# Optimization experiments

Measured on AMD Instinct MI355X. Metric: run time of the kernel, lower is better.

Reference implementation:

```python
import jax, jax.numpy as jnp
import numpy as np

EMBED_DIM = 512
NUM_HEADS = 8
HEAD_DIM = EMBED_DIM // NUM_HEADS


def setup_inputs() -> dict:
    key = jax.random.key(0)
    kx, kq, kk, kv, ko = jax.random.split(key, 5)
    B, T, C = 2, 4096, EMBED_DIM
    s = 1.0 / np.sqrt(C)  # torch Linear default init scale (uniform); use scaled normal
    return {
        "x": jax.random.normal(kx, (B, T, C), dtype=jnp.float32),
        "Wq": jax.random.normal(kq, (C, C), dtype=jnp.float32) * s,
        "Wk": jax.random.normal(kk, (C, C), dtype=jnp.float32) * s,
        "Wv": jax.random.normal(kv, (C, C), dtype=jnp.float32) * s,
        "Wo": jax.random.normal(ko, (C, C), dtype=jnp.float32) * s,
    }


def reference(x, Wq, Wk, Wv, Wo):
    B, T, C = x.shape
    H, D = NUM_HEADS, HEAD_DIM

    def split_heads(t):
        return t.reshape(B, T, H, D).transpose(0, 2, 1, 3)  # [B,H,T,D]

    # nn.Linear: y = x @ W^T
    Q = split_heads(x @ Wq.T)
    K = split_heads(x @ Wk.T)
    V = split_heads(x @ Wv.T)

    scale = jnp.sqrt(jnp.asarray(D, dtype=x.dtype))
    scores = jnp.einsum("bhqd,bhkd->bhqk", Q, K) / scale  # [B,H,T,T]
    causal = jnp.tril(jnp.ones((T, T), dtype=bool))
    scores = jnp.where(causal, scores, -jnp.inf)
    weights = jax.nn.softmax(scores, axis=-1)
    out = jnp.einsum("bhqk,bhkd->bhqd", weights, V)  # [B,H,T,D]
    out = out.transpose(0, 2, 1, 3).reshape(B, T, C)
    return out @ Wo.T
```

## Files before the change

### kernel.cpp

```cpp
#include <hip/hip_runtime.h>
#include <stdint.h>

#define B_DIM 2
#define T_DIM 4096
#define C_DIM 512
#define H_DIM 8
#define D_DIM 64
#define M_DIM (B_DIM * T_DIM)

typedef __attribute__((ext_vector_type(8))) short bf16x8;
typedef __attribute__((ext_vector_type(4))) float f32x4;
typedef __attribute__((ext_vector_type(4))) short short4v;

__device__ inline unsigned short f2bf(float f) {
    union { float f; uint32_t u; } v; v.f = f;
    uint32_t r = v.u + 0x7fffu + ((v.u >> 16) & 1u);
    return (unsigned short)(r >> 16);
}

__device__ inline uint32_t cvtpk(float a, float b) {
    uint32_t r;
    asm("v_cvt_pk_bf16_f32 %0, %1, %2" : "=v"(r) : "v"(a), "v"(b));
    return r;
}

__device__ inline float fexp2(float x) {
    float r;
    asm("v_exp_f32 %0, %1" : "=v"(r) : "v"(x));
    return r;
}

__device__ inline float bf2f(unsigned short u) {
    union { uint32_t u; float f; } v; v.u = (uint32_t)u << 16; return v.f;
}

__global__ __launch_bounds__(256) void cvt_kernel(const float* __restrict__ in,
                                                  unsigned short* __restrict__ out, int n) {
    int i = (blockIdx.x * 256 + threadIdx.x) * 4;
    if (i >= n) return;
    float4 v = *(const float4*)(in + i);
    uint2 o;
    o.x = cvtpk(v.x, v.y);
    o.y = cvtpk(v.z, v.w);
    *(uint2*)(out + i) = o;
}

__global__ __launch_bounds__(256) void cvt_w_kernel(const float* __restrict__ Wq,
                                                    const float* __restrict__ Wk,
                                                    const float* __restrict__ Wv,
                                                    const float* __restrict__ Wo,
                                                    unsigned short* __restrict__ out) {
    const int widx = blockIdx.x >> 8;
    const float* src = (widx == 0) ? Wq : (widx == 1) ? Wk : (widx == 2) ? Wv : Wo;
    const int i = ((blockIdx.x & 255) * 256 + threadIdx.x) * 4;
    float4 v = *(const float4*)(src + i);
    uint2 o;
    o.x = cvtpk(v.x, v.y);
    o.y = cvtpk(v.z, v.w);
    *(uint2*)(out + (size_t)widx * C_DIM * C_DIM + i) = o;
}

__global__ __launch_bounds__(256, 2) void gemm_qkv(const unsigned short* __restrict__ A,
                                                   const unsigned short* __restrict__ Wb,
                                                   unsigned short* __restrict__ Qh,
                                                   unsigned short* __restrict__ Kh,
                                                   unsigned short* __restrict__ Vt) {
    const int tid  = threadIdx.x;
    const int wave = tid >> 6;
    const int lane = tid & 63;
    const int g    = lane >> 4;
    const int lr   = lane & 15;
    const int rowB = blockIdx.x * 128;
    const int col0 = blockIdx.y * 128;
    const int z    = blockIdx.z;
    const unsigned short* W = Wb + (size_t)z * C_DIM * C_DIM;

    __shared__ unsigned short As[2][128][40];
    __shared__ unsigned short Bs[2][128][40];

    const int sr = tid >> 1;
    const int sc = (tid & 1) * 16;

    f32x4 acc[2][8];
#pragma unroll
    for (int r = 0; r < 2; ++r)
#pragma unroll
        for (int i = 0; i < 8; ++i) acc[r][i] = (f32x4){0.f, 0.f, 0.f, 0.f};

    const unsigned short* Ag = A + (size_t)(rowB + sr) * C_DIM + sc;
    const unsigned short* Bg = W + (size_t)(col0 + sr) * C_DIM + sc;

    *(bf16x8*)&As[0][sr][sc]     = *(const bf16x8*)(Ag);
    *(bf16x8*)&As[0][sr][sc + 8] = *(const bf16x8*)(Ag + 8);
    *(bf16x8*)&Bs[0][sr][sc]     = *(const bf16x8*)(Bg);
    *(bf16x8*)&Bs[0][sr][sc + 8] = *(const bf16x8*)(Bg + 8);
    __syncthreads();

    int cur = 0;
#pragma unroll 1
    for (int kk = 0; kk < C_DIM; kk += 32) {
        const bool hn = (kk + 32 < C_DIM);
        bf16x8 na0, na1, nb0, nb1;
        if (hn) {
            na0 = *(const bf16x8*)(Ag + kk + 32);
            na1 = *(const bf16x8*)(Ag + kk + 40);
            nb0 = *(const bf16x8*)(Bg + kk + 32);
            nb1 = *(const bf16x8*)(Bg + kk + 40);
        }

        bf16x8 a0 = *(const bf16x8*)&As[cur][wave * 32 + lr][g * 8];
        bf16x8 a1 = *(const bf16x8*)&As[cur][wave * 32 + 16 + lr][g * 8];
#pragma unroll
        for (int nt = 0; nt < 8; ++nt) {
            bf16x8 b = *(const bf16x8*)&Bs[cur][nt * 16 + lr][g * 8];
            acc[0][nt] = __builtin_amdgcn_mfma_f32_16x16x32_bf16(a0, b, acc[0][nt], 0, 0, 0);
            acc[1][nt] = __builtin_amdgcn_mfma_f32_16x16x32_bf16(a1, b, acc[1][nt], 0, 0, 0);
        }

        if (hn) {
            *(bf16x8*)&As[cur ^ 1][sr][sc]     = na0;
            *(bf16x8*)&As[cur ^ 1][sr][sc + 8] = na1;
            *(bf16x8*)&Bs[cur ^ 1][sr][sc]     = nb0;
            *(bf16x8*)&Bs[cur ^ 1][sr][sc + 8] = nb1;
        }
        __syncthreads();
        cur ^= 1;
    }

    const int row0 = rowB + wave * 32;
    unsigned short* Oqk = (z == 0) ? Qh : Kh;
#pragma unroll
    for (int ar = 0; ar < 2; ++ar) {
        const int rowb = row0 + ar * 16;
#pragma unroll
        for (int nt = 0; nt < 8; ++nt) {
            const int n = col0 + nt * 16 + lr;
            const int h = n >> 6, d = n & 63;
            if (z < 2) {
#pragma unroll
                for (int j = 0; j < 4; ++j) {
                    int m = rowb + g * 4 + j;
                    int b = m >> 12, t = m & (T_DIM - 1);
                    Oqk[((size_t)(b * H_DIM + h) * T_DIM + t) * D_DIM + d] = f2bf(acc[ar][nt][j]);
                }
            } else {
                int m = rowb + g * 4;
                int b = m >> 12, t = m & (T_DIM - 1);
                int tp = (t & ~31) | (((t >> 2) & 3) << 3) | (((t >> 4) & 1) << 2);
                short4v pack;
#pragma unroll
                for (int j = 0; j < 4; ++j) pack[j] = (short)f2bf(acc[ar][nt][j]);
                *(short4v*)(Vt + ((size_t)(b * H_DIM + h) * D_DIM + d) * T_DIM + tp) = pack;
            }
        }
    }
}

__global__ __launch_bounds__(256, 2) void gemm_out(const unsigned short* __restrict__ A,
                                                   const unsigned short* __restrict__ W,
                                                   float* __restrict__ O) {
    const int tid  = threadIdx.x;
    const int wave = tid >> 6;
    const int lane = tid & 63;
    const int g    = lane >> 4;
    const int lr   = lane & 15;
    const int rowB = blockIdx.x * 128;
    const int col0 = blockIdx.y * 128;

    __shared__ unsigned short As[2][128][40];
    __shared__ unsigned short Bs[2][128][40];

    const int sr = tid >> 1;
    const int sc = (tid & 1) * 16;

    f32x4 acc[2][8];
#pragma unroll
    for (int r = 0; r < 2; ++r)
#pragma unroll
        for (int i = 0; i < 8; ++i) acc[r][i] = (f32x4){0.f, 0.f, 0.f, 0.f};

    const unsigned short* Ag = A + (size_t)(rowB + sr) * C_DIM + sc;
    const unsigned short* Bg = W + (size_t)(col0 + sr) * C_DIM + sc;

    *(bf16x8*)&As[0][sr][sc]     = *(const bf16x8*)(Ag);
    *(bf16x8*)&As[0][sr][sc + 8] = *(const bf16x8*)(Ag + 8);
    *(bf16x8*)&Bs[0][sr][sc]     = *(const bf16x8*)(Bg);
    *(bf16x8*)&Bs[0][sr][sc + 8] = *(const bf16x8*)(Bg + 8);
    __syncthreads();

    int cur = 0;
#pragma unroll 1
    for (int kk = 0; kk < C_DIM; kk += 32) {
        const bool hn = (kk + 32 < C_DIM);
        bf16x8 na0, na1, nb0, nb1;
        if (hn) {
            na0 = *(const bf16x8*)(Ag + kk + 32);
            na1 = *(const bf16x8*)(Ag + kk + 40);
            nb0 = *(const bf16x8*)(Bg + kk + 32);
            nb1 = *(const bf16x8*)(Bg + kk + 40);
        }

        bf16x8 a0 = *(const bf16x8*)&As[cur][wave * 32 + lr][g * 8];
        bf16x8 a1 = *(const bf16x8*)&As[cur][wave * 32 + 16 + lr][g * 8];
#pragma unroll
        for (int nt = 0; nt < 8; ++nt) {
            bf16x8 b = *(const bf16x8*)&Bs[cur][nt * 16 + lr][g * 8];
            acc[0][nt] = __builtin_amdgcn_mfma_f32_16x16x32_bf16(a0, b, acc[0][nt], 0, 0, 0);
            acc[1][nt] = __builtin_amdgcn_mfma_f32_16x16x32_bf16(a1, b, acc[1][nt], 0, 0, 0);
        }

        if (hn) {
            *(bf16x8*)&As[cur ^ 1][sr][sc]     = na0;
            *(bf16x8*)&As[cur ^ 1][sr][sc + 8] = na1;
            *(bf16x8*)&Bs[cur ^ 1][sr][sc]     = nb0;
            *(bf16x8*)&Bs[cur ^ 1][sr][sc + 8] = nb1;
        }
        __syncthreads();
        cur ^= 1;
    }

    const int row0 = rowB + wave * 32;
#pragma unroll
    for (int ar = 0; ar < 2; ++ar) {
        const int rowb = row0 + ar * 16;
#pragma unroll
        for (int nt = 0; nt < 8; ++nt) {
            const int n = col0 + nt * 16 + lr;
#pragma unroll
            for (int j = 0; j < 4; ++j) {
                int m = rowb + g * 4 + j;
                O[(size_t)m * C_DIM + n] = acc[ar][nt][j];
            }
        }
    }
}

__global__ __launch_bounds__(256, 2) void attn_lds(const unsigned short* __restrict__ Qh,
                                                   const unsigned short* __restrict__ Kh,
                                                   const unsigned short* __restrict__ Vt,
                                                   unsigned short* __restrict__ pO,
                                                   float* __restrict__ pl) {
    const int tid  = threadIdx.x;
    const int wave = tid >> 6;
    const int lane = tid & 63;
    const int g    = lane >> 4;
    const int lr   = lane & 15;
    const int srow = (tid >> 3) & 31;
    const int scol = (tid & 7) * 8;
    const int bid  = blockIdx.x;
    const int bh   = bid & 15;
    const int half = (bid >> 4) & 1;
    const int pr   = bid >> 5;

    const unsigned short* Qp = Qh + (size_t)bh * T_DIM * D_DIM;
    const unsigned short* Kp = Kh + (size_t)bh * T_DIM * D_DIM;
    const unsigned short* Vp = Vt + (size_t)bh * D_DIM * T_DIM;

    const float KC = 0.125f * 1.44269504f;
    const short oneb = (short)0x3F80;
    const bf16x8 ones = {oneb, oneb, oneb, oneb, oneb, oneb, oneb, oneb};

    __shared__ unsigned short Kb[2][2][64][72];
    __shared__ unsigned short Vb[2][2][64][72];

#pragma unroll 1
    for (int t = 0; t < 2; ++t) {
        const int qt = t ? (31 - pr) : pr;
        const int qw = qt * 128 + wave * 32;
        const int kvend_w = qw + 32;
        const int kvend_b = qt * 128 + 128;
        const int kvstart = half * 128;

        bf16x8 qf[2][2];
#pragma unroll
        for (int h = 0; h < 2; ++h)
#pragma unroll
            for (int dh = 0; dh < 2; ++dh)
                qf[h][dh] = *(const bf16x8*)(Qp + (size_t)(qw + h * 16 + lr) * D_DIM + dh * 32 + g * 8);

        f32x4 oacc[2][4];
        f32x4 o5[2];
#pragma unroll
        for (int h = 0; h < 2; ++h) {
#pragma unroll
            for (int d0 = 0; d0 < 4; ++d0) oacc[h][d0] = (f32x4){0.f, 0.f, 0.f, 0.f};
            o5[h] = (f32x4){0.f, 0.f, 0.f, 0.f};
        }

#pragma unroll
        for (int s = 0; s < 2; ++s) {
            const int kb = kvstart + s * 64;
            const unsigned short* Ks = Kp + (size_t)(kb + srow) * D_DIM + scol;
            bf16x8 k0 = *(const bf16x8*)(Ks);
            bf16x8 k1 = *(const bf16x8*)(Ks + 32 * D_DIM);
            const unsigned short* Vs = Vp + (size_t)srow * T_DIM + kb + scol;
            bf16x8 v0 = *(const bf16x8*)(Vs);
            bf16x8 v1 = *(const bf16x8*)(Vs + 32 * T_DIM);
            *(bf16x8*)&Kb[0][s][srow][scol]      = k0;
            *(bf16x8*)&Kb[0][s][srow + 32][scol] = k1;
            *(bf16x8*)&Vb[0][s][srow][scol]      = v0;
            *(bf16x8*)&Vb[0][s][srow + 32][scol] = v1;
        }
        __syncthreads();

        int cur = 0;
#pragma unroll 1
        for (int kv0 = kvstart; kv0 < kvend_b; kv0 += 256) {
            const int kvn = kv0 + 256;
            const bool hn = kvn < kvend_b;

            bf16x8 gk[2][2], gv[2][2];
            if (hn) {
#pragma unroll
                for (int s = 0; s < 2; ++s) {
                    const int kb = kvn + s * 64;
                    const unsigned short* Ks = Kp + (size_t)(kb + srow) * D_DIM + scol;
                    gk[s][0] = *(const bf16x8*)(Ks);
                    gk[s][1] = *(const bf16x8*)(Ks + 32 * D_DIM);
                    const unsigned short* Vs = Vp + (size_t)srow * T_DIM + kb + scol;
                    gv[s][0] = *(const bf16x8*)(Vs);
                    gv[s][1] = *(const bf16x8*)(Vs + 32 * T_DIM);
                }
            }

#pragma unroll 1
            for (int sub = 0; sub < 2; ++sub) {
                const int kvu = kv0 + sub * 64;
                if (kvu < kvend_w) {
                    bf16x8 kc8[4][2], vf[2][4];
#pragma unroll
                    for (int i = 0; i < 4; ++i)
#pragma unroll
                        for (int dh = 0; dh < 2; ++dh)
                            kc8[i][dh] = *(const bf16x8*)&Kb[cur][sub][i * 16 + lr][dh * 32 + g * 8];
#pragma unroll
                    for (int kh = 0; kh < 2; ++kh)
#pragma unroll
                        for (int d0 = 0; d0 < 4; ++d0)
                            vf[kh][d0] = *(const bf16x8*)&Vb[cur][sub][d0 * 16 + lr][kh * 32 + g * 8];

                    f32x4 s[2][4];
#pragma unroll
                    for (int h = 0; h < 2; ++h)
#pragma unroll
                        for (int i = 0; i < 4; ++i) s[h][i] = (f32x4){0.f, 0.f, 0.f, 0.f};
#pragma unroll
                    for (int i = 0; i < 4; ++i) {
                        s[0][i] = __builtin_amdgcn_mfma_f32_16x16x32_bf16(kc8[i][0], qf[0][0], s[0][i], 0, 0, 0);
                        s[0][i] = __builtin_amdgcn_mfma_f32_16x16x32_bf16(kc8[i][1], qf[0][1], s[0][i], 0, 0, 0);
                        s[1][i] = __builtin_amdgcn_mfma_f32_16x16x32_bf16(kc8[i][0], qf[1][0], s[1][i], 0, 0, 0);
                        s[1][i] = __builtin_amdgcn_mfma_f32_16x16x32_bf16(kc8[i][1], qf[1][1], s[1][i], 0, 0, 0);
                    }

                    const bool maskit = (kvu + 63 > qw);
#pragma unroll
                    for (int h = 0; h < 2; ++h) {
                        const int qh = qw + h * 16 + lr;
                        float p[16];
                        if (maskit) {
#pragma unroll
                            for (int i = 0; i < 4; ++i)
#pragma unroll
                                for (int j = 0; j < 4; ++j) {
                                    int kva = kvu + i * 16 + g * 4 + j;
                                    float zz = (kva > qh) ? -1e30f : s[h][i][j];
                                    p[i * 4 + j] = fexp2(zz * KC);
                                }
                        } else {
#pragma unroll
                            for (int i = 0; i < 4; ++i)
#pragma unroll
                                for (int j = 0; j < 4; ++j)
                                    p[i * 4 + j] = fexp2(s[h][i][j] * KC);
                        }

                        union { bf16x8 v; uint32_t w[4]; } pf0, pf1;
#pragma unroll
                        for (int w = 0; w < 4; ++w) pf0.w[w] = cvtpk(p[2 * w], p[2 * w + 1]);
#pragma unroll
                        for (int w = 0; w < 4; ++w) pf1.w[w] = cvtpk(p[8 + 2 * w], p[9 + 2 * w]);

#pragma unroll
                        for (int d0 = 0; d0 < 4; ++d0)
                            oacc[h][d0] = __builtin_amdgcn_mfma_f32_16x16x32_bf16(vf[0][d0], pf0.v, oacc[h][d0], 0, 0, 0);
                        o5[h] = __builtin_amdgcn_mfma_f32_16x16x32_bf16(ones, pf0.v, o5[h], 0, 0, 0);
#pragma unroll
                        for (int d0 = 0; d0 < 4; ++d0)
                            oacc[h][d0] = __builtin_amdgcn_mfma_f32_16x16x32_bf16(vf[1][d0], pf1.v, oacc[h][d0], 0, 0, 0);
                        o5[h] = __builtin_amdgcn_mfma_f32_16x16x32_bf16(ones, pf1.v, o5[h], 0, 0, 0);
                    }
                }
            }

            if (hn) {
#pragma unroll
                for (int s = 0; s < 2; ++s) {
                    *(bf16x8*)&Kb[cur ^ 1][s][srow][scol]      = gk[s][0];
                    *(bf16x8*)&Kb[cur ^ 1][s][srow + 32][scol] = gk[s][1];
                    *(bf16x8*)&Vb[cur ^ 1][s][srow][scol]      = gv[s][0];
                    *(bf16x8*)&Vb[cur ^ 1][s][srow + 32][scol] = gv[s][1];
                }
            }
            __syncthreads();
            cur ^= 1;
        }

        const size_t hb = ((size_t)(half * 16 + bh)) * T_DIM;
#pragma unroll
        for (int h = 0; h < 2; ++h) {
            const int row = qw + h * 16 + lr;
            unsigned short* orow = pO + (hb + row) * D_DIM;
#pragma unroll
            for (int d0 = 0; d0 < 4; ++d0) {
                uint2 st;
                st.x = cvtpk(oacc[h][d0][0], oacc[h][d0][1]);
                st.y = cvtpk(oacc[h][d0][2], oacc[h][d0][3]);
                *(uint2*)(orow + d0 * 16 + g * 4) = st;
            }
            if (g == 0) pl[hb + row] = o5[h][0];
        }
        __syncthreads();
    }
}

__global__ __launch_bounds__(256) void attn_merge(const unsigned short* __restrict__ pO,
                                                  const float* __restrict__ pl,
                                                  unsigned short* __restrict__ attnb) {
    const int c = blockIdx.x * 256 + threadIdx.x;
    const int row = c >> 3;
    const int d = (c & 7) * 8;
    const int bh = row >> 12, r = row & 4095;
    const size_t HS = (size_t)16 * T_DIM * D_DIM;

    const size_t pbase = (size_t)row * D_DIM + d;
    bf16x8 a = *(const bf16x8*)(pO + pbase);
    bf16x8 b = *(const bf16x8*)(pO + HS + pbase);
    const float inv = 1.0f / (pl[row] + pl[(HS / D_DIM) + row]);

    union { bf16x8 v; uint32_t w[4]; } o;
#pragma unroll
    for (int i = 0; i < 4; ++i) {
        float e0 = (bf2f((unsigned short)a[2 * i])     + bf2f((unsigned short)b[2 * i]))     * inv;
        float e1 = (bf2f((unsigned short)a[2 * i + 1]) + bf2f((unsigned short)b[2 * i + 1])) * inv;
        o.w[i] = cvtpk(e0, e1);
    }
    const int bb = bh >> 3, hh = bh & 7;
    *(bf16x8*)(attnb + ((size_t)(bb * T_DIM + r)) * C_DIM + hh * D_DIM + d) = o.v;
}

extern "C" void kernel_launch(void* const* d_in, const int* in_sizes, int n_in,
                              void* d_out, int out_size, void* d_ws, size_t ws_size,
                              hipStream_t stream) {
    const float* x  = (const float*)d_in[0];
    const float* Wq = (const float*)d_in[1];
    const float* Wk = (const float*)d_in[2];
    const float* Wv = (const float*)d_in[3];
    const float* Wo = (const float*)d_in[4];

    char* ws = (char*)d_ws;
    unsigned short* xb    = (unsigned short*)(ws + 0);
    unsigned short* Wb    = (unsigned short*)(ws + 8388608);
    unsigned short* Qh    = (unsigned short*)(ws + 10485760);
    unsigned short* Kh    = (unsigned short*)(ws + 18874368);
    unsigned short* Vt    = (unsigned short*)(ws + 27262976);
    unsigned short* attnb = (unsigned short*)(ws + 35651584);
    unsigned short* pO    = (unsigned short*)(ws + 44040192);
    float*          pl    = (float*)         (ws + 60817408);

    const int nX = M_DIM * C_DIM;

    cvt_kernel<<<nX / 4 / 256, 256, 0, stream>>>(x, xb, nX);
    cvt_w_kernel<<<1024, 256, 0, stream>>>(Wq, Wk, Wv, Wo, Wb);

    dim3 gq(M_DIM / 128, C_DIM / 128, 3);
    gemm_qkv<<<gq, 256, 0, stream>>>(xb, Wb, Qh, Kh, Vt);

    attn_lds<<<512, 256, 0, stream>>>(Qh, Kh, Vt, pO, pl);
    attn_merge<<<2048, 256, 0, stream>>>(pO, pl, attnb);

    gemm_out<<<dim3(M_DIM / 128, C_DIM / 128), 256, 0, stream>>>(attnb, Wb + 3 * C_DIM * C_DIM, (float*)d_out);
}
```

Baseline: 98.35 us.

## Fuse split-KV merge into output GEMM and prescale Q by softmax constant

Removes the separate attn_merge kernel. gemm_out now reads both partial attention outputs and their row sums, normalises them and converts to bf16 while loading its A tiles, which removes one launch and an intermediate buffer round-trip. The softmax scale times log2(e) is also folded into Q at projection time, saving a multiply per score in the attention loop. In exchange, the merge work is repeated across the four column blocks of gemm_out, adding redundant global reads of pO and pl. Rounding Q after scaling also changes bf16 precision slightly.

```diff
diff --git a/kernel.cpp b/kernel.cpp
--- a/kernel.cpp
+++ b/kernel.cpp
@@ -33,6 +33,8 @@
 __device__ inline float bf2f(unsigned short u) {
     union { uint32_t u; float f; } v; v.u = (uint32_t)u << 16; return v.f;
 }
+
+#define KCONST 0.1803368801111204f
 
 __global__ __launch_bounds__(256) void cvt_kernel(const float* __restrict__ in,
                                                   unsigned short* __restrict__ out, int n) {
@@ -129,6 +131,7 @@
 
     const int row0 = rowB + wave * 32;
     unsigned short* Oqk = (z == 0) ? Qh : Kh;
+    const float qs = (z == 0) ? KCONST : 1.0f;
 #pragma unroll
     for (int ar = 0; ar < 2; ++ar) {
         const int rowb = row0 + ar * 16;
@@ -141,7 +144,7 @@
                 for (int j = 0; j < 4; ++j) {
                     int m = rowb + g * 4 + j;
                     int b = m >> 12, t = m & (T_DIM - 1);
-                    Oqk[((size_t)(b * H_DIM + h) * T_DIM + t) * D_DIM + d] = f2bf(acc[ar][nt][j]);
+                    Oqk[((size_t)(b * H_DIM + h) * T_DIM + t) * D_DIM + d] = f2bf(acc[ar][nt][j] * qs);
                 }
             } else {
                 int m = rowb + g * 4;
@@ -156,7 +159,30 @@
     }
 }
 
-__global__ __launch_bounds__(256, 2) void gemm_out(const unsigned short* __restrict__ A,
+__device__ inline void mergeA16(const unsigned short* __restrict__ pO,
+                                const float* __restrict__ pl,
+                                int rowid, int d, bf16x8* out0, bf16x8* out1) {
+    const size_t HS = (size_t)65536 * 64;
+    const size_t pb = (size_t)rowid * 64 + d;
+    bf16x8 lo0 = *(const bf16x8*)(pO + pb);
+    bf16x8 lo1 = *(const bf16x8*)(pO + pb + 8);
+    bf16x8 hi0 = *(const bf16x8*)(pO + HS + pb);
+    bf16x8 hi1 = *(const bf16x8*)(pO + HS + pb + 8);
+    const float linv = 1.0f / (pl[rowid] + pl[65536 + rowid]);
+    union { bf16x8 v; uint32_t w[4]; } a, b;
+#pragma unroll
+    for (int i = 0; i < 4; ++i) {
+        a.w[i] = cvtpk((bf2f((unsigned short)lo0[2 * i])     + bf2f((unsigned short)hi0[2 * i]))     * linv,
+                       (bf2f((unsigned short)lo0[2 * i + 1]) + bf2f((unsigned short)hi0[2 * i + 1])) * linv);
+        b.w[i] = cvtpk((bf2f((unsigned short)lo1[2 * i])     + bf2f((unsigned short)hi1[2 * i]))     * linv,
+                       (bf2f((unsigned short)lo1[2 * i + 1]) + bf2f((unsigned short)hi1[2 * i + 1])) * linv);
+    }
+    *out0 = a.v;
+    *out1 = b.v;
+}
+
+__global__ __launch_bounds__(256, 2) void gemm_out(const unsigned short* __restrict__ pO,
+                                                   const float* __restrict__ pl,
                                                    const unsigned short* __restrict__ W,
                                                    float* __restrict__ O) {
     const int tid  = threadIdx.x;
@@ -172,6 +198,8 @@
 
     const int sr = tid >> 1;
     const int sc = (tid & 1) * 16;
+    const int m  = rowB + sr;
+    const int bb = m >> 12, tt = m & (T_DIM - 1);
 
     f32x4 acc[2][8];
 #pragma unroll
@@ -179,11 +207,16 @@
 #pragma unroll
         for (int i = 0; i < 8; ++i) acc[r][i] = (f32x4){0.f, 0.f, 0.f, 0.f};
 
-    const unsigned short* Ag = A + (size_t)(rowB + sr) * C_DIM + sc;
     const unsigned short* Bg = W + (size_t)(col0 + sr) * C_DIM + sc;
 
-    *(bf16x8*)&As[0][sr][sc]     = *(const bf16x8*)(Ag);
-    *(bf16x8*)&As[0][sr][sc + 8] = *(const bf16x8*)(Ag + 8);
+    {
+        const int c = sc;
+        const int rowid = ((bb * 8 + (c >> 6)) << 12) | tt;
+        bf16x8 a0, a1;
+        mergeA16(pO, pl, rowid, c & 63, &a0, &a1);
+        *(bf16x8*)&As[0][sr][sc]     = a0;
+        *(bf16x8*)&As[0][sr][sc + 8] = a1;
+    }
     *(bf16x8*)&Bs[0][sr][sc]     = *(const bf16x8*)(Bg);
     *(bf16x8*)&Bs[0][sr][sc + 8] = *(const bf16x8*)(Bg + 8);
     __syncthreads();
@@ -194,8 +227,9 @@
         const bool hn = (kk + 32 < C_DIM);
         bf16x8 na0, na1, nb0, nb1;
         if (hn) {
-            na0 = *(const bf16x8*)(Ag + kk + 32);
-            na1 = *(const bf16x8*)(Ag + kk + 40);
+            const int c = kk + 32 + sc;
+            const int rowid = ((bb * 8 + (c >> 6)) << 12) | tt;
+            mergeA16(pO, pl, rowid, c & 63, &na0, &na1);
             nb0 = *(const bf16x8*)(Bg + kk + 32);
             nb1 = *(const bf16x8*)(Bg + kk + 40);
         }
@@ -228,8 +262,8 @@
             const int n = col0 + nt * 16 + lr;
 #pragma unroll
             for (int j = 0; j < 4; ++j) {
-                int m = rowb + g * 4 + j;
-                O[(size_t)m * C_DIM + n] = acc[ar][nt][j];
+                int mm = rowb + g * 4 + j;
+                O[(size_t)mm * C_DIM + n] = acc[ar][nt][j];
             }
         }
     }
@@ -256,7 +290,6 @@
     const unsigned short* Kp = Kh + (size_t)bh * T_DIM * D_DIM;
     const unsigned short* Vp = Vt + (size_t)bh * D_DIM * T_DIM;
 
-    const float KC = 0.125f * 1.44269504f;
     const short oneb = (short)0x3F80;
     const bf16x8 ones = {oneb, oneb, oneb, oneb, oneb, oneb, oneb, oneb};
 
@@ -364,14 +397,14 @@
                                 for (int j = 0; j < 4; ++j) {
                                     int kva = kvu + i * 16 + g * 4 + j;
                                     float zz = (kva > qh) ? -1e30f : s[h][i][j];
-                                    p[i * 4 + j] = fexp2(zz * KC);
+                                    p[i * 4 + j] = fexp2(zz);
                                 }
                         } else {
 #pragma unroll
                             for (int i = 0; i < 4; ++i)
 #pragma unroll
                                 for (int j = 0; j < 4; ++j)
-                                    p[i * 4 + j] = fexp2(s[h][i][j] * KC);
+                                    p[i * 4 + j] = fexp2(s[h][i][j]);
                         }
 
                         union { bf16x8 v; uint32_t w[4]; } pf0, pf1;
@@ -421,31 +454,6 @@
         }
         __syncthreads();
     }
-}
-
-__global__ __launch_bounds__(256) void attn_merge(const unsigned short* __restrict__ pO,
-                                                  const float* __restrict__ pl,
-                                                  unsigned short* __restrict__ attnb) {
-    const int c = blockIdx.x * 256 + threadIdx.x;
-    const int row = c >> 3;
-    const int d = (c & 7) * 8;
-    const int bh = row >> 12, r = row & 4095;
-    const size_t HS = (size_t)16 * T_DIM * D_DIM;
-
-    const size_t pbase = (size_t)row * D_DIM + d;
-    bf16x8 a = *(const bf16x8*)(pO + pbase);
-    bf16x8 b = *(const bf16x8*)(pO + HS + pbase);
-    const float inv = 1.0f / (pl[row] + pl[(HS / D_DIM) + row]);
-
-    union { bf16x8 v; uint32_t w[4]; } o;
-#pragma unroll
-    for (int i = 0; i < 4; ++i) {
-        float e0 = (bf2f((unsigned short)a[2 * i])     + bf2f((unsigned short)b[2 * i]))     * inv;
-        float e1 = (bf2f((unsigned short)a[2 * i + 1]) + bf2f((unsigned short)b[2 * i + 1])) * inv;
-        o.w[i] = cvtpk(e0, e1);
-    }
-    const int bb = bh >> 3, hh = bh & 7;
-    *(bf16x8*)(attnb + ((size_t)(bb * T_DIM + r)) * C_DIM + hh * D_DIM + d) = o.v;
 }
 
 extern "C" void kernel_launch(void* const* d_in, const int* in_sizes, int n_in,
@@ -463,7 +471,6 @@
     unsigned short* Qh    = (unsigned short*)(ws + 10485760);
     unsigned short* Kh    = (unsigned short*)(ws + 18874368);
     unsigned short* Vt    = (unsigned short*)(ws + 27262976);
-    unsigned short* attnb = (unsigned short*)(ws + 35651584);
     unsigned short* pO    = (unsigned short*)(ws + 44040192);
     float*          pl    = (float*)         (ws + 60817408);
 
@@ -476,7 +483,6 @@
     gemm_qkv<<<gq, 256, 0, stream>>>(xb, Wb, Qh, Kh, Vt);
 
     attn_lds<<<512, 256, 0, stream>>>(Qh, Kh, Vt, pO, pl);
-    attn_merge<<<2048, 256, 0, stream>>>(pO, pl, attnb);
-
-    gemm_out<<<dim3(M_DIM / 128, C_DIM / 128), 256, 0, stream>>>(attnb, Wb + 3 * C_DIM * C_DIM, (float*)d_out);
-}
+
+    gemm_out<<<dim3(M_DIM / 128, C_DIM / 128), 256, 0, stream>>>(pO, pl, Wb + 3 * C_DIM * C_DIM, (float*)d_out);
+}
```

Result: no change. 99.68 us (+1.4%).
